# Kernel tuning notes

Measured on AMD Instinct MI355X. Metric: run time of the kernel, lower is better.

Reference implementation:

```python
import jax, jax.numpy as jnp
import numpy as np

TEMPERATURE = 0.5
N_NODES = 100000
N_EDGES = 3200000
D = 32


def setup_inputs() -> dict:
    key = jax.random.key(0)
    ks = jax.random.split(key, 8)
    node_reps = jax.random.normal(ks[0], (N_NODES, D), dtype=jnp.float32)
    edge_reps = jax.random.normal(ks[1], (N_EDGES, D), dtype=jnp.float32)
    graph_rep = jax.random.normal(ks[2], (D,), dtype=jnp.float32)
    subgraph_rep = jax.random.normal(ks[3], (D,), dtype=jnp.float32)
    W = jax.random.normal(ks[4], (3 * D, D), dtype=jnp.float32) / np.sqrt(3 * D)
    b = jax.random.normal(ks[5], (D,), dtype=jnp.float32) * 0.01
    edge_index = jax.random.randint(ks[6], (2, N_EDGES), 0, N_NODES, dtype=jnp.int64)
    selection = jax.random.randint(ks[7], (N_EDGES,), 0, 2) > 0
    return {
        "node_reps": node_reps,
        "edge_reps": edge_reps,
        "graph_rep": graph_rep,
        "subgraph_rep": subgraph_rep,
        "W": W,
        "b": b,
        "edge_index": edge_index,
        "selection": selection,
    }


def reference(node_reps, edge_reps, graph_rep, subgraph_rep, W, b, edge_index, selection):
    # Gather endpoint node reps per edge: [E, 32] each
    src = node_reps[edge_index[0]]
    dst = node_reps[edge_index[1]]
    # Concat -> [E, 96], Linear + ELU -> [E, 32]
    h = jnp.concatenate([src, dst, edge_reps], axis=1)
    edge_action_reps = jax.nn.elu(h @ W + b)
    # State scores: [E] = [E,32] @ [32]
    state_prob = edge_action_reps @ (graph_rep - subgraph_rep)
    # Mask already-selected edges to the global minimum, then softmax with temperature
    min_prob = jnp.min(state_prob)
    state_prob = jnp.where(selection, min_prob, state_prob)
    return jax.nn.softmax(state_prob[None, :] / TEMPERATURE, axis=1)
```

## Files before the change

kernel.cpp:

```cpp
#include <hip/hip_runtime.h>
#include <hip/hip_bf16.h>
#include <stdint.h>

#define DD 32
#define KH 96


__device__ __forceinline__ uint32_t fkey(float f) {
    uint32_t b = __float_as_uint(f);
    return (b & 0x80000000u) ? ~b : (b | 0x80000000u);
}
__device__ __forceinline__ float funkey(uint32_t k) {
    uint32_t b = (k & 0x80000000u) ? (k & 0x7FFFFFFFu) : ~k;
    return __uint_as_float(b);
}
__device__ __forceinline__ float bflo(uint32_t w) { return __uint_as_float(w << 16); }
__device__ __forceinline__ float bfhi(uint32_t w) { return __uint_as_float(w & 0xFFFF0000u); }

__global__ void k_init(const void* W, const void* bias, const void* g, const void* sg,
                       const void* ei, const void* sel,
                       uint32_t* hdr, float* Wf, float* bf, float* vf, int E, int N) {
    int t = threadIdx.x;
    __shared__ int sh_i32, sh_gt1, sh_odd, sh_f32;
    if (t == 0) { sh_i32 = 0; sh_gt1 = 0; sh_odd = 0; sh_f32 = 0; }
    __syncthreads();

    const uint16_t* wb = (const uint16_t*)W;
    for (int i = t; i < KH * DD; i += 256) {
        float x = bflo((uint32_t)wb[i]);
        if (!(fabsf(x) < 1e4f)) sh_f32 = 1;
    }
    const long long* ell = (const long long*)ei;
    int ns = 2048 < E ? 2048 : E;
    for (int i = t; i < ns; i += 256) {
        long long v = ell[i];
        if (v < 0 || v >= (long long)N) sh_i32 = 1;
    }
    const uint32_t* sw = (const uint32_t*)sel;
    int ns2 = 2048 < E / 4 ? 2048 : E / 4;
    for (int i = t; i < ns2; i += 256) {
        uint32_t v = sw[i];
        if (v > 1u) sh_gt1 = 1;
        if (v != 0u && (i & 1)) sh_odd = 1;
    }
    __syncthreads();
    int fmode = sh_f32;

    for (int i = t; i < KH * DD; i += 256)
        Wf[i] = fmode ? ((const float*)W)[i] : bflo((uint32_t)wb[i]);
    for (int i = t; i < DD; i += 256) {
        bf[i] = fmode ? ((const float*)bias)[i] : bflo((uint32_t)((const uint16_t*)bias)[i]);
        float gv = fmode ? ((const float*)g)[i]  : bflo((uint32_t)((const uint16_t*)g)[i]);
        float sv = fmode ? ((const float*)sg)[i] : bflo((uint32_t)((const uint16_t*)sg)[i]);
        vf[i] = gv - sv;
    }
    if (t == 0) {
        hdr[0] = (uint32_t)sh_i32;
        hdr[1] = sh_gt1 ? 2u : (sh_odd ? 1u : 0u);
        hdr[2] = (uint32_t)fmode;
        hdr[3] = 0xFFFFFFFFu;
        hdr[4] = 0u;
        hdr[5] = 0u;
        hdr[6] = 0u;
    }
}

__device__ __forceinline__ void load_row(const void* base, size_t row, int fmode, float* h) {
    if (fmode) {
        const float4* q = (const float4*)((const float*)base + row * DD);
        #pragma unroll
        for (int t = 0; t < 8; ++t) {
            float4 u = q[t];
            h[t * 4 + 0] = u.x; h[t * 4 + 1] = u.y; h[t * 4 + 2] = u.z; h[t * 4 + 3] = u.w;
        }
    } else {
        const uint4* q = (const uint4*)((const uint16_t*)base + row * DD);
        #pragma unroll
        for (int t = 0; t < 4; ++t) {
            uint4 u = q[t];
            uint32_t w0 = u.x, w1 = u.y, w2 = u.z, w3 = u.w;
            h[t * 8 + 0] = bflo(w0); h[t * 8 + 1] = bfhi(w0);
            h[t * 8 + 2] = bflo(w1); h[t * 8 + 3] = bfhi(w1);
            h[t * 8 + 4] = bflo(w2); h[t * 8 + 5] = bfhi(w2);
            h[t * 8 + 6] = bflo(w3); h[t * 8 + 7] = bfhi(w3);
        }
    }
}

__device__ __forceinline__ bool fetch_sel(const void* sel, int mode, int e) {
    if (mode == 2) return ((const uint8_t*)sel)[e] != 0;
    if (mode == 1) return ((const int*)sel)[e] != 0;
    return ((const long long*)sel)[e] != 0;
}

__device__ __forceinline__ float compute_sp(int e, const void* node, const void* edge,
                                            const void* ei, int idx_mode, int fmode,
                                            const float* Wf, const float* bf, const float* vf,
                                            int E, int N) {
    long long si, di;
    if (idx_mode) { si = ((const int*)ei)[e]; di = ((const int*)ei)[E + e]; }
    else          { si = ((const long long*)ei)[e]; di = ((const long long*)ei)[E + e]; }
    int s0 = (int)si, d0 = (int)di;
    s0 = s0 < 0 ? 0 : (s0 >= N ? N - 1 : s0);
    d0 = d0 < 0 ? 0 : (d0 >= N ? N - 1 : d0);

    float h[KH];
    load_row(node, (size_t)s0, fmode, h);
    load_row(node, (size_t)d0, fmode, h + 32);
    load_row(edge, (size_t)e, fmode, h + 64);

    float sp = 0.f;
    for (int j = 0; j < DD; ++j) {
        float a0 = bf[j], a1 = 0.f, a2 = 0.f, a3 = 0.f;
        #pragma unroll
        for (int k = 0; k < KH; k += 4) {
            a0 = fmaf(h[k + 0], Wf[(k + 0) * DD + j], a0);
            a1 = fmaf(h[k + 1], Wf[(k + 1) * DD + j], a1);
            a2 = fmaf(h[k + 2], Wf[(k + 2) * DD + j], a2);
            a3 = fmaf(h[k + 3], Wf[(k + 3) * DD + j], a3);
        }
        float acc = (a0 + a1) + (a2 + a3);
        float act = acc > 0.f ? acc : (__expf(acc) - 1.f);
        sp = fmaf(act, vf[j], sp);
    }
    return sp;
}

template <int STORE>
__global__ __launch_bounds__(256) void k_pass1(const void* node, const void* edge, const void* ei,
                                               const void* sel, uint32_t* hdr, const float* Wf,
                                               const float* bf, const float* vf, float* sp_arr,
                                               int E, int N) {
    int e = blockIdx.x * 256 + threadIdx.x;
    int idx_mode = (int)hdr[0], sel_mode = (int)hdr[1], fmode = (int)hdr[2];
    float sp = 0.f;
    bool selv = true;
    bool valid = e < E;
    if (valid) {
        sp = compute_sp(e, node, edge, ei, idx_mode, fmode, Wf, bf, vf, E, N);
        if (STORE) sp_arr[e] = sp;
        selv = fetch_sel(sel, sel_mode, e);
    }
    float mn = valid ? sp : __builtin_inff();
    float mx = (valid && !selv) ? sp : -__builtin_inff();
    uint32_t c = (valid && !selv) ? 1u : 0u;
    #pragma unroll
    for (int o = 32; o >= 1; o >>= 1) {
        mn = fminf(mn, __shfl_xor(mn, o));
        mx = fmaxf(mx, __shfl_xor(mx, o));
        c += __shfl_xor(c, o);
    }
    __shared__ float smn[4], smx[4];
    __shared__ uint32_t sc[4];
    int wid = threadIdx.x >> 6, lane = threadIdx.x & 63;
    if (lane == 0) { smn[wid] = mn; smx[wid] = mx; sc[wid] = c; }
    __syncthreads();
    if (threadIdx.x == 0) {
        for (int w = 1; w < 4; ++w) { mn = fminf(mn, smn[w]); mx = fmaxf(mx, smx[w]); c += sc[w]; }
        atomicMin(&hdr[3], fkey(mn));
        atomicMax(&hdr[4], fkey(mx));
        if (c) atomicAdd(&hdr[5], c);
    }
}

template <int LOAD>
__global__ __launch_bounds__(256) void k_pass2(const void* node, const void* edge, const void* ei,
                                               const void* sel, uint32_t* hdr, const float* Wf,
                                               const float* bf, const float* vf,
                                               const float* sp_arr, int E, int N) {
    int e = blockIdx.x * 256 + threadIdx.x;
    int idx_mode = (int)hdr[0], sel_mode = (int)hdr[1], fmode = (int)hdr[2];
    float mn = funkey(hdr[3]);
    uint32_t cnt = hdr[5];
    float M = cnt ? funkey(hdr[4]) : mn;
    float p = 0.f;
    if (e < E) {
        float sp = LOAD ? sp_arr[e]
                        : compute_sp(e, node, edge, ei, idx_mode, fmode, Wf, bf, vf, E, N);
        bool selv = fetch_sel(sel, sel_mode, e);
        float masked = selv ? mn : sp;
        p = __expf((masked - M) * 2.0f);
    }
    #pragma unroll
    for (int o = 32; o >= 1; o >>= 1) p += __shfl_xor(p, o);
    __shared__ float sps[4];
    int wid = threadIdx.x >> 6, lane = threadIdx.x & 63;
    if (lane == 0) sps[wid] = p;
    __syncthreads();
    if (threadIdx.x == 0) {
        p += sps[1] + sps[2] + sps[3];
        atomicAdd((float*)&hdr[6], p);
    }
}

template <int LOAD>
__global__ __launch_bounds__(256) void k_pass3(const void* node, const void* edge, const void* ei,
                                               const void* sel, const uint32_t* hdr, const float* Wf,
                                               const float* bf, const float* vf,
                                               const float* sp_arr, void* out, int E, int N) {
    int e = blockIdx.x * 256 + threadIdx.x;
    if (e >= E) return;
    int idx_mode = (int)hdr[0], sel_mode = (int)hdr[1], fmode = (int)hdr[2];
    float mn = funkey(hdr[3]);
    uint32_t cnt = hdr[5];
    float M = cnt ? funkey(hdr[4]) : mn;
    float S = __uint_as_float(hdr[6]);
    float sp = LOAD ? sp_arr[e]
                    : compute_sp(e, node, edge, ei, idx_mode, fmode, Wf, bf, vf, E, N);
    bool selv = fetch_sel(sel, sel_mode, e);
    float masked = selv ? mn : sp;
    float r = __expf((masked - M) * 2.0f) / S;
    if (fmode) ((float*)out)[e] = r;
    else       ((__hip_bfloat16*)out)[e] = __float2bfloat16(r);
}

extern "C" void kernel_launch(void* const* d_in, const int* in_sizes, int n_in,
                              void* d_out, int out_size, void* d_ws, size_t ws_size,
                              hipStream_t stream) {
    int N = in_sizes[0] / DD;
    int E = in_sizes[1] / DD;
    const void* node = d_in[0];
    const void* edge = d_in[1];
    const void* g    = d_in[2];
    const void* sg   = d_in[3];
    const void* W    = d_in[4];
    const void* bias = d_in[5];
    const void* ei   = d_in[6];
    const void* sel  = d_in[7];

    uint8_t* ws = (uint8_t*)d_ws;
    uint32_t* hdr = (uint32_t*)ws;
    float* Wf = (float*)(ws + 256);
    float* bf = (float*)(ws + 256 + 12288);
    float* vf = (float*)(ws + 256 + 12288 + 128);
    float* sp_arr = (float*)(ws + 16384);
    bool store = ws_size >= (size_t)16384 + (size_t)E * sizeof(float);

    int grid = (E + 255) / 256;
    k_init<<<1, 256, 0, stream>>>(W, bias, g, sg, ei, sel, hdr, Wf, bf, vf, E, N);
    if (store) {
        k_pass1<1><<<grid, 256, 0, stream>>>(node, edge, ei, sel, hdr, Wf, bf, vf, sp_arr, E, N);
        k_pass2<1><<<grid, 256, 0, stream>>>(node, edge, ei, sel, hdr, Wf, bf, vf, sp_arr, E, N);
        k_pass3<1><<<grid, 256, 0, stream>>>(node, edge, ei, sel, hdr, Wf, bf, vf, sp_arr, d_out, E, N);
    } else {
        k_pass1<0><<<grid, 256, 0, stream>>>(node, edge, ei, sel, hdr, Wf, bf, vf, sp_arr, E, N);
        k_pass2<0><<<grid, 256, 0, stream>>>(node, edge, ei, sel, hdr, Wf, bf, vf, sp_arr, E, N);
        k_pass3<0><<<grid, 256, 0, stream>>>(node, edge, ei, sel, hdr, Wf, bf, vf, sp_arr, d_out, E, N);
    }
}
```

Before: 1.154 ms.

## Stage weights in LDS, restructure edge MLP loop, drop recompute fallback

Pass 1 now copies the 96x32 weight matrix, bias and score vector into shared memory once per block. It computes all 32 output accumulators together with an outer-product loop that reads float4 weight rows and overlaps the next row's gather with compute. The recompute-on-no-workspace path is removed; scores instead go to the output buffer when workspace is short. The goal is fewer scalar global weight loads and better instruction-level parallelism, at the cost of more registers (32 accumulators plus two 32-float buffers) and lower occupancy.

After: 1.142 ms. About the same (-1.1%).

```diff
diff --git a/kernel.cpp b/kernel.cpp
--- a/kernel.cpp
+++ b/kernel.cpp
@@ -16,6 +16,11 @@
 }
 __device__ __forceinline__ float bflo(uint32_t w) { return __uint_as_float(w << 16); }
 __device__ __forceinline__ float bfhi(uint32_t w) { return __uint_as_float(w & 0xFFFF0000u); }
+__device__ __forceinline__ uint16_t f2bf(float v) {
+    uint32_t u = __float_as_uint(v);
+    uint32_t r = (u + 0x7FFFu + ((u >> 16) & 1u)) >> 16;
+    return (uint16_t)r;
+}
 
 __global__ void k_init(const void* W, const void* bias, const void* g, const void* sg,
                        const void* ei, const void* sel,
@@ -65,82 +70,124 @@
     }
 }
 
-__device__ __forceinline__ void load_row(const void* base, size_t row, int fmode, float* h) {
+__device__ __forceinline__ void loadrow(const char* __restrict__ p, int fmode, float* h) {
     if (fmode) {
-        const float4* q = (const float4*)((const float*)base + row * DD);
+        const float4* q = (const float4*)p;
         #pragma unroll
         for (int t = 0; t < 8; ++t) {
             float4 u = q[t];
             h[t * 4 + 0] = u.x; h[t * 4 + 1] = u.y; h[t * 4 + 2] = u.z; h[t * 4 + 3] = u.w;
         }
     } else {
-        const uint4* q = (const uint4*)((const uint16_t*)base + row * DD);
+        const uint4* q = (const uint4*)p;
         #pragma unroll
         for (int t = 0; t < 4; ++t) {
             uint4 u = q[t];
-            uint32_t w0 = u.x, w1 = u.y, w2 = u.z, w3 = u.w;
-            h[t * 8 + 0] = bflo(w0); h[t * 8 + 1] = bfhi(w0);
-            h[t * 8 + 2] = bflo(w1); h[t * 8 + 3] = bfhi(w1);
-            h[t * 8 + 4] = bflo(w2); h[t * 8 + 5] = bfhi(w2);
-            h[t * 8 + 6] = bflo(w3); h[t * 8 + 7] = bfhi(w3);
-        }
-    }
-}
-
-__device__ __forceinline__ bool fetch_sel(const void* sel, int mode, int e) {
+            h[t * 8 + 0] = bflo(u.x); h[t * 8 + 1] = bfhi(u.x);
+            h[t * 8 + 2] = bflo(u.y); h[t * 8 + 3] = bfhi(u.y);
+            h[t * 8 + 4] = bflo(u.z); h[t * 8 + 5] = bfhi(u.z);
+            h[t * 8 + 6] = bflo(u.w); h[t * 8 + 7] = bfhi(u.w);
+        }
+    }
+}
+
+__device__ __forceinline__ bool fetch_sel(const char* sel, int mode, int e) {
     if (mode == 2) return ((const uint8_t*)sel)[e] != 0;
     if (mode == 1) return ((const int*)sel)[e] != 0;
     return ((const long long*)sel)[e] != 0;
 }
 
-__device__ __forceinline__ float compute_sp(int e, const void* node, const void* edge,
-                                            const void* ei, int idx_mode, int fmode,
-                                            const float* Wf, const float* bf, const float* vf,
-                                            int E, int N) {
+__device__ __forceinline__ void sp_store(float* __restrict__ ws_sp, void* __restrict__ out,
+                                         int use_ws, int fmode, int e, float v) {
+    if (use_ws) ws_sp[e] = v;
+    else if (fmode) ((float*)out)[e] = v;
+    else ((uint16_t*)out)[e] = f2bf(v);
+}
+__device__ __forceinline__ float sp_load(const float* __restrict__ ws_sp, const void* __restrict__ out,
+                                         int use_ws, int fmode, int e) {
+    if (use_ws) return ws_sp[e];
+    if (fmode) return ((const float*)out)[e];
+    return bflo((uint32_t)((const uint16_t*)out)[e]);
+}
+
+__global__ __launch_bounds__(256) void k_pass1(
+    const char* __restrict__ node, const char* __restrict__ edgep,
+    const char* __restrict__ ei, const char* __restrict__ sel,
+    uint32_t* __restrict__ hdr, const float* __restrict__ Wf,
+    const float* __restrict__ bf, const float* __restrict__ vf,
+    float* __restrict__ ws_sp, void* __restrict__ out,
+    int use_ws, int E, int N) {
+    __shared__ __align__(16) float Ws[KH * DD];
+    __shared__ float bs[DD], vs[DD];
+    for (int i = threadIdx.x; i < KH * DD; i += 256) Ws[i] = Wf[i];
+    if (threadIdx.x < DD) { bs[threadIdx.x] = bf[threadIdx.x]; vs[threadIdx.x] = vf[threadIdx.x]; }
+    const int idx_mode = (int)hdr[0];
+    const int sel_mode = (int)hdr[1];
+    const int fmode    = (int)hdr[2];
+    __syncthreads();
+
+    int e = blockIdx.x * 256 + threadIdx.x;
+    bool valid = e < E;
+    int ec = valid ? e : E - 1;
+
     long long si, di;
-    if (idx_mode) { si = ((const int*)ei)[e]; di = ((const int*)ei)[E + e]; }
-    else          { si = ((const long long*)ei)[e]; di = ((const long long*)ei)[E + e]; }
-    int s0 = (int)si, d0 = (int)di;
-    s0 = s0 < 0 ? 0 : (s0 >= N ? N - 1 : s0);
-    d0 = d0 < 0 ? 0 : (d0 >= N ? N - 1 : d0);
-
-    float h[KH];
-    load_row(node, (size_t)s0, fmode, h);
-    load_row(node, (size_t)d0, fmode, h + 32);
-    load_row(edge, (size_t)e, fmode, h + 64);
+    if (idx_mode) { si = ((const int*)ei)[ec]; di = ((const int*)ei)[E + ec]; }
+    else          { si = ((const long long*)ei)[ec]; di = ((const long long*)ei)[(size_t)E + ec]; }
+    int s0 = (int)si; s0 = s0 < 0 ? 0 : (s0 >= N ? N - 1 : s0);
+    int d0 = (int)di; d0 = d0 < 0 ? 0 : (d0 >= N ? N - 1 : d0);
+
+    size_t rb = fmode ? 128 : 64;
+    const char* p0 = node  + (size_t)s0 * rb;
+    const char* p1 = node  + (size_t)d0 * rb;
+    const char* p2 = edgep + (size_t)ec * rb;
+
+    float acc[DD];
+    #pragma unroll
+    for (int j = 0; j < DD; ++j) acc[j] = bs[j];
+
+    float hh[32], hn[32];
+    loadrow(p0, fmode, hh);
+
+    #pragma unroll 1
+    for (int r = 0; r < 3; ++r) {
+        if (r < 2) {
+            const char* pn = (r == 0) ? p1 : p2;
+            loadrow(pn, fmode, hn);
+        }
+        const float* wb = &Ws[r * 32 * DD];
+        #pragma unroll
+        for (int k = 0; k < 32; ++k) {
+            float hk = hh[k];
+            const float4* wp = (const float4*)(wb + k * DD);
+            #pragma unroll
+            for (int j4 = 0; j4 < 8; ++j4) {
+                float4 w = wp[j4];
+                acc[j4 * 4 + 0] = fmaf(hk, w.x, acc[j4 * 4 + 0]);
+                acc[j4 * 4 + 1] = fmaf(hk, w.y, acc[j4 * 4 + 1]);
+                acc[j4 * 4 + 2] = fmaf(hk, w.z, acc[j4 * 4 + 2]);
+                acc[j4 * 4 + 3] = fmaf(hk, w.w, acc[j4 * 4 + 3]);
+            }
+        }
+        if (r < 2) {
+            #pragma unroll
+            for (int k = 0; k < 32; ++k) hh[k] = hn[k];
+        }
+    }
 
     float sp = 0.f;
+    #pragma unroll
     for (int j = 0; j < DD; ++j) {
-        float a0 = bf[j], a1 = 0.f, a2 = 0.f, a3 = 0.f;
-        #pragma unroll
-        for (int k = 0; k < KH; k += 4) {
-            a0 = fmaf(h[k + 0], Wf[(k + 0) * DD + j], a0);
-            a1 = fmaf(h[k + 1], Wf[(k + 1) * DD + j], a1);
-            a2 = fmaf(h[k + 2], Wf[(k + 2) * DD + j], a2);
-            a3 = fmaf(h[k + 3], Wf[(k + 3) * DD + j], a3);
-        }
-        float acc = (a0 + a1) + (a2 + a3);
-        float act = acc > 0.f ? acc : (__expf(acc) - 1.f);
-        sp = fmaf(act, vf[j], sp);
-    }
-    return sp;
-}
-
-template <int STORE>
-__global__ __launch_bounds__(256) void k_pass1(const void* node, const void* edge, const void* ei,
-                                               const void* sel, uint32_t* hdr, const float* Wf,
-                                               const float* bf, const float* vf, float* sp_arr,
-                                               int E, int N) {
-    int e = blockIdx.x * 256 + threadIdx.x;
-    int idx_mode = (int)hdr[0], sel_mode = (int)hdr[1], fmode = (int)hdr[2];
-    float sp = 0.f;
+        float a = acc[j];
+        float act = a > 0.f ? a : (__expf(a) - 1.f);
+        sp = fmaf(act, vs[j], sp);
+    }
+
     bool selv = true;
-    bool valid = e < E;
     if (valid) {
-        sp = compute_sp(e, node, edge, ei, idx_mode, fmode, Wf, bf, vf, E, N);
-        if (STORE) sp_arr[e] = sp;
+        sp_store(ws_sp, out, use_ws, fmode, e, sp);
         selv = fetch_sel(sel, sel_mode, e);
     }
+
     float mn = valid ? sp : __builtin_inff();
     float mx = (valid && !selv) ? sp : -__builtin_inff();
     uint32_t c = (valid && !selv) ? 1u : 0u;
@@ -163,20 +210,18 @@
     }
 }
 
-template <int LOAD>
-__global__ __launch_bounds__(256) void k_pass2(const void* node, const void* edge, const void* ei,
-                                               const void* sel, uint32_t* hdr, const float* Wf,
-                                               const float* bf, const float* vf,
-                                               const float* sp_arr, int E, int N) {
+__global__ __launch_bounds__(256) void k_pass2(
+    const char* __restrict__ sel, uint32_t* __restrict__ hdr,
+    const float* __restrict__ ws_sp, const void* __restrict__ out,
+    int use_ws, int E) {
     int e = blockIdx.x * 256 + threadIdx.x;
-    int idx_mode = (int)hdr[0], sel_mode = (int)hdr[1], fmode = (int)hdr[2];
+    int sel_mode = (int)hdr[1], fmode = (int)hdr[2];
     float mn = funkey(hdr[3]);
     uint32_t cnt = hdr[5];
     float M = cnt ? funkey(hdr[4]) : mn;
     float p = 0.f;
     if (e < E) {
-        float sp = LOAD ? sp_arr[e]
-                        : compute_sp(e, node, edge, ei, idx_mode, fmode, Wf, bf, vf, E, N);
+        float sp = sp_load(ws_sp, out, use_ws, fmode, e);
         bool selv = fetch_sel(sel, sel_mode, e);
         float masked = selv ? mn : sp;
         p = __expf((masked - M) * 2.0f);
@@ -193,25 +238,23 @@
     }
 }
 
-template <int LOAD>
-__global__ __launch_bounds__(256) void k_pass3(const void* node, const void* edge, const void* ei,
-                                               const void* sel, const uint32_t* hdr, const float* Wf,
-                                               const float* bf, const float* vf,
-                                               const float* sp_arr, void* out, int E, int N) {
+__global__ __launch_bounds__(256) void k_pass3(
+    const char* __restrict__ sel, const uint32_t* __restrict__ hdr,
+    const float* __restrict__ ws_sp, void* __restrict__ out,
+    int use_ws, int E) {
     int e = blockIdx.x * 256 + threadIdx.x;
     if (e >= E) return;
-    int idx_mode = (int)hdr[0], sel_mode = (int)hdr[1], fmode = (int)hdr[2];
+    int sel_mode = (int)hdr[1], fmode = (int)hdr[2];
     float mn = funkey(hdr[3]);
     uint32_t cnt = hdr[5];
     float M = cnt ? funkey(hdr[4]) : mn;
     float S = __uint_as_float(hdr[6]);
-    float sp = LOAD ? sp_arr[e]
-                    : compute_sp(e, node, edge, ei, idx_mode, fmode, Wf, bf, vf, E, N);
+    float sp = sp_load(ws_sp, out, use_ws, fmode, e);
     bool selv = fetch_sel(sel, sel_mode, e);
     float masked = selv ? mn : sp;
     float r = __expf((masked - M) * 2.0f) / S;
     if (fmode) ((float*)out)[e] = r;
-    else       ((__hip_bfloat16*)out)[e] = __float2bfloat16(r);
+    else       ((uint16_t*)out)[e] = f2bf(r);
 }
 
 extern "C" void kernel_launch(void* const* d_in, const int* in_sizes, int n_in,
@@ -234,17 +277,13 @@
     float* bf = (float*)(ws + 256 + 12288);
     float* vf = (float*)(ws + 256 + 12288 + 128);
     float* sp_arr = (float*)(ws + 16384);
-    bool store = ws_size >= (size_t)16384 + (size_t)E * sizeof(float);
+    int use_ws = (ws_size >= (size_t)16384 + (size_t)E * sizeof(float)) ? 1 : 0;
 
     int grid = (E + 255) / 256;
     k_init<<<1, 256, 0, stream>>>(W, bias, g, sg, ei, sel, hdr, Wf, bf, vf, E, N);
-    if (store) {
-        k_pass1<1><<<grid, 256, 0, stream>>>(node, edge, ei, sel, hdr, Wf, bf, vf, sp_arr, E, N);
-        k_pass2<1><<<grid, 256, 0, stream>>>(node, edge, ei, sel, hdr, Wf, bf, vf, sp_arr, E, N);
-        k_pass3<1><<<grid, 256, 0, stream>>>(node, edge, ei, sel, hdr, Wf, bf, vf, sp_arr, d_out, E, N);
-    } else {
-        k_pass1<0><<<grid, 256, 0, stream>>>(node, edge, ei, sel, hdr, Wf, bf, vf, sp_arr, E, N);
-        k_pass2<0><<<grid, 256, 0, stream>>>(node, edge, ei, sel, hdr, Wf, bf, vf, sp_arr, E, N);
-        k_pass3<0><<<grid, 256, 0, stream>>>(node, edge, ei, sel, hdr, Wf, bf, vf, sp_arr, d_out, E, N);
-    }
-}
+    k_pass1<<<grid, 256, 0, stream>>>((const char*)node, (const char*)edge, (const char*)ei,
+                                      (const char*)sel, hdr, Wf, bf, vf, sp_arr, d_out,
+                                      use_ws, E, N);
+    k_pass2<<<grid, 256, 0, stream>>>((const char*)sel, hdr, sp_arr, d_out, use_ws, E);
+    k_pass3<<<grid, 256, 0, stream>>>((const char*)sel, hdr, sp_arr, d_out, use_ws, E);
+}
```
